# Kernel tuning notes

Hardware: AMD Instinct MI355X
Metric: run time of the kernel (lower is better)

The kernel has to match this reference:

```python
import jax, jax.numpy as jnp
from jax import lax
import numpy as np

B = 16384
D = 32
N_HEADS = 4


def _piece_table():
    base = np.zeros((7, 4, 4), np.int32)
    cells = [
        [(1, 0), (1, 1), (1, 2), (1, 3)],  # I
        [(1, 1), (1, 2), (2, 1), (2, 2)],  # O
        [(1, 1), (2, 0), (2, 1), (2, 2)],  # T
        [(1, 1), (1, 2), (2, 0), (2, 1)],  # S
        [(1, 0), (1, 1), (2, 1), (2, 2)],  # Z
        [(1, 0), (2, 0), (2, 1), (2, 2)],  # J
        [(1, 2), (2, 0), (2, 1), (2, 2)],  # L
    ]
    for i, cs in enumerate(cells):
        for (r, c) in cs:
            base[i, r, c] = 1
    rots = np.stack([np.stack([np.rot90(base[i], k) for k in range(4)]) for i in range(7)])
    p = np.concatenate([rots, np.zeros((1, 4, 4, 4), np.int32)], 0)  # [8,4,4,4]
    return jnp.asarray(p)


def setup_inputs() -> dict:
    key = jax.random.key(0)
    ks = jax.random.split(key, 24)

    def ri(k, n, lo, hi):
        return jax.random.randint(k, (B, n), lo, hi, dtype=jnp.int32)

    t = jnp.concatenate([
        ri(ks[0], 1, 0, 10),   # col0 feature
        ri(ks[1], 1, 2, 8),
        ri(ks[2], 1, 0, 10),   # col2 y pos
        ri(ks[3], 1, 0, 8),    # col3 drop dist
        ri(ks[4], 1, 0, 4),    # col4 rotation
        ri(ks[5], 3, 0, 10),   # cols5-7
        ri(ks[6], 1, 0, 7),    # col8 piece id
        ri(ks[7], 6, 0, 7),    # cols9-14 hold/next
        ri(ks[8], 7, 0, 10),   # cols15-21
        ri(ks[9], 210, 0, 2),  # cols22-231 board
    ], axis=1)

    s = 0.05
    rn = lambda k, shp: jax.random.normal(k, shp, jnp.float32) * s
    return {
        "t": t,
        "piece_table": _piece_table(),
        "conv1_w": rn(ks[10], (6, 3, 5, 5)), "conv1_b": rn(ks[11], (6,)),
        "conv2_w": rn(ks[12], (16, 6, 5, 5)), "conv2_b": rn(ks[13], (16,)),
        "conv3_w": rn(ks[14], (64, 16, 3, 1)), "conv3_b": rn(ks[15], (64,)),
        "lfc1_w": rn(ks[16], (32, 64)), "lfc1_b": rn(ks[17], (32,)),
        "fc_w": rn(ks[18], (32, 8)), "fc_b": rn(ks[19], (32,)),
        "emb": rn(ks[20], (8, D)),
        "in_proj_w": rn(ks[21], (3 * D, D)), "in_proj_b": jnp.zeros((3 * D,), jnp.float32),
        "out_proj_w": rn(ks[22], (D, D)), "out_proj_b": jnp.zeros((D,), jnp.float32),
    }


def _avgpool2(x):
    b, c, h, w = x.shape
    h2, w2 = h // 2, w // 2
    return x[:, :, :h2 * 2, :w2 * 2].reshape(b, c, h2, 2, w2, 2).mean((3, 5))


def _lenet(x, w1, b1, w2, b2, w3, b3, fw, fb):
    dn = ("NCHW", "OIHW", "NCHW")
    x = jax.nn.relu(lax.conv_general_dilated(x, w1, (1, 1), ((2, 2), (2, 2)), dimension_numbers=dn) + b1[None, :, None, None])
    x = _avgpool2(x)                                   # [B,6,11,6]
    x = jax.nn.relu(lax.conv_general_dilated(x, w2, (1, 1), ((0, 0), (0, 0)), dimension_numbers=dn) + b2[None, :, None, None])
    x = _avgpool2(x)                                   # [B,16,3,1]
    x = jax.nn.relu(lax.conv_general_dilated(x, w3, (1, 1), ((0, 0), (0, 0)), dimension_numbers=dn) + b3[None, :, None, None])
    x = x.reshape(-1, 64)
    return jax.nn.relu(x @ fw.T + fb)                  # [B,32]


def _pe():
    pos = jnp.array([0, 0, 1, 2, 3, 4, 5], jnp.float32)[:, None]
    div = jnp.exp(jnp.arange(0, D, 2, dtype=jnp.float32) * (-jnp.log(10000.0) / D))
    s, c = jnp.sin(pos * div), jnp.cos(pos * div)      # [7,16] each
    return jnp.stack([s, c], -1).reshape(7, D)         # interleaved sin/cos


def _mha(q_in, kv, in_w, in_b, out_w, out_b):
    qw, kw, vw = in_w[:D], in_w[D:2 * D], in_w[2 * D:]
    qb, kb, vb = in_b[:D], in_b[D:2 * D], in_b[2 * D:]
    b, lq, _ = q_in.shape
    hd = D // N_HEADS
    q = (q_in @ qw.T + qb).reshape(b, lq, N_HEADS, hd)
    k = (kv @ kw.T + kb).reshape(b, -1, N_HEADS, hd)
    v = (kv @ vw.T + vb).reshape(b, -1, N_HEADS, hd)
    scores = jnp.einsum("bqhd,bkhd->bhqk", q, k) / jnp.sqrt(jnp.float32(hd))
    w = jax.nn.softmax(scores, axis=-1)
    o = jnp.einsum("bhqk,bkhd->bqhd", w, v).reshape(b, lq, D)
    return o @ out_w.T + out_b


def reference(t, piece_table, conv1_w, conv1_b, conv2_w, conv2_b, conv3_w, conv3_b,
              lfc1_w, lfc1_b, fc_w, fc_b, emb, in_proj_w, in_proj_b, out_proj_w, out_proj_b):
    bsz = t.shape[0]
    board = jnp.zeros((bsz, 3, 21, 10), jnp.float32)
    board = board.at[:, 0].set(t[:, 22:232].astype(jnp.float32).reshape(bsz, 21, 10))

    # gather piece grid, extract the 4 filled cells per sample in row-major order
    pieces = piece_table[t[:, 8], t[:, 4]].reshape(bsz, 16)        # [B,16] in {0,1}
    idx = jnp.argsort(1 - pieces, axis=1, stable=True)[:, :4]      # first 4 ones, scan order
    cy, cx = idx // 4, idx % 4
    x = cx + t[:, 1][:, None] - 2
    y = cy + t[:, 2][:, None]
    ny = y + t[:, 3][:, None]
    mask = (y >= 0) & (ny >= 0)
    br = jnp.arange(bsz, dtype=jnp.int32)[:, None]
    y_m = jnp.where(mask, y, -1)
    ny_m = jnp.where(mask, ny, -1)
    board = board.at[br, 1, y_m, x].set(1.0, mode="drop")
    board = board.at[br, 2, ny_m, x].set(1.0, mode="drop")

    board = jnp.pad(board, ((0, 0), (0, 0), (0, 1), (1, 1)), constant_values=1.0)  # [B,3,22,12]

    t9 = jnp.where((t[:, 9] != -1) & (t[:, 6] != 0), t[:, 9], 7)
    hold_next = jnp.concatenate([t[:, 8:9], t9[:, None], t[:, 10:15]], axis=1)     # [B,7]

    b2 = _lenet(board, conv1_w, conv1_b, conv2_w, conv2_b, conv3_w, conv3_b, lfc1_w, lfc1_b)  # [B,32]
    bkv = b2[:, None, :]                                            # [B,1,32]
    p = emb[hold_next] + _pe()[None]                                # [B,7,32]
    a = _mha(p, bkv, in_proj_w, in_proj_b, out_proj_w, out_proj_b)  # [B,7,32]

    xf = jax.nn.relu(t[:, :8].astype(jnp.float32) @ fc_w.T + fc_b)  # [B,32]
    out = jnp.concatenate([xf, a.mean(axis=1), b2], axis=1)         # [B,96]
    return (out, board)
```

## Files before the change

### kernel.cpp

```cpp
#include <hip/hip_runtime.h>
#include <cstddef>


#define BATCH 16384
#define SPB   4
#define NBLK  (BATCH / SPB)
#define RS    18
#define SBE_SZ 432
#define P1OFF  432
#define PCSOFF 800
#define SS2    816

__global__ __launch_bounds__(256)
void cborder_kernel(const float* __restrict__ w1, float* __restrict__ cb)
{
  int i = blockIdx.x * 256 + threadIdx.x;
  if (i >= 1584) return;
  int p = i / 6, o = i - p * 6;
  int y0 = p / 12, x0 = p - y0 * 12;
  float acc = 0.f;
#pragma unroll
  for (int dy = 0; dy < 5; ++dy)
#pragma unroll
    for (int dx = 0; dx < 5; ++dx) {
      int pr = y0 + dy - 2, pc = x0 + dx - 2;
      if (pr >= 0 && pr < 22 && pc >= 0 && pc < 12 &&
          (pr == 21 || pc == 0 || pc == 11)) {
        int k = dy * 5 + dx;
        acc += w1[(o * 3 + 0) * 25 + k] + w1[(o * 3 + 1) * 25 + k]
             + w1[(o * 3 + 2) * 25 + k];
      }
    }
  cb[p * 6 + o] = acc;
}

__global__ __launch_bounds__(256)
void board_model_kernel(const int* __restrict__ t,
                        const int* __restrict__ piece_table,
                        const float* __restrict__ w1, const float* __restrict__ b1,
                        const float* __restrict__ w2, const float* __restrict__ b2w,
                        const float* __restrict__ w3, const float* __restrict__ b3,
                        const float* __restrict__ wf1, const float* __restrict__ bf1,
                        const float* __restrict__ fcw, const float* __restrict__ fcb,
                        const float* __restrict__ ipw, const float* __restrict__ ipb,
                        const float* __restrict__ opw, const float* __restrict__ opb,
                        const float* __restrict__ cbg,
                        float* __restrict__ out,
                        float* __restrict__ out_board)
{
  __shared__ __align__(16) float scr[SPB * SS2];
  __shared__ float w1L[300];
  __shared__ float cbL[1440];

  const int tid  = threadIdx.x;
  const int lane = tid & 63;
  const int wv   = tid >> 6;
  const int bb   = blockIdx.x * SPB;

  for (int i = tid; i < 300; i += 256)
    w1L[i] = w1[(i / 50) * 75 + 25 + (i % 50)];
  for (int i = tid; i < 1440; i += 256) cbL[i] = cbg[i];

  {
    float* W = &scr[wv * SS2];
    int*   pcs = (int*)&scr[wv * SS2 + PCSOFF];
    const int* tr = t + (size_t)(bb + wv) * 232;

    float4* W4 = (float4*)W;
    for (int i = lane; i < 108; i += 64) W4[i] = float4{0.f, 0.f, 0.f, 0.f};

    for (int i = lane; i < 210; i += 64) {
      int r = i / 10, b = i - r * 10;
      W[(r + 2) * RS + b + 5] = (float)tr[22 + i];
    }

    if (lane < 4) {
      const int* pt = piece_table + (tr[8] * 4 + tr[4]) * 16;
      int sel = -1, n1 = 0;
#pragma unroll
      for (int j = 0; j < 16; ++j) { if (pt[j]) { if (n1 == lane) sel = j; ++n1; } }
      if (sel < 0) {
        int n0 = 0, want = lane - n1;
#pragma unroll
        for (int j = 0; j < 16; ++j) if (!pt[j]) { if (n0 == want) { sel = j; break; } ++n0; }
      }
      int cy = sel >> 2, cx = sel & 3;
      int x  = cx + tr[1] - 2;
      int y  = cy + tr[2];
      int ny = y + tr[3];
      bool mask = (y >= 0) && (ny >= 0);
      bool xok  = (x >= 0) && (x < 10);
      bool v1 = mask && xok && (y < 21);
      bool v2 = mask && xok && (ny < 21);
      pcs[2 * lane + 0]       = v1 ? y  : -100;
      pcs[2 * lane + 1]       = x + 1;
      pcs[2 * (lane + 4)]     = v2 ? ny : -100;
      pcs[2 * (lane + 4) + 1] = x + 1;
    }
    __builtin_amdgcn_wave_barrier();

    float* ob = out_board + (size_t)(bb + wv) * 792;
    for (int v = lane; v < 198; v += 64) {
      int j0 = v * 4;
      int ch = j0 / 264, rem = j0 - ch * 264;
      int r = rem / 12, c = rem - r * 12;
      float val[4];
      if (ch == 0) {
#pragma unroll
        for (int d = 0; d < 4; ++d) {
          int cd = c + d;
          val[d] = (r == 21 || cd == 0 || cd == 11) ? 1.f
                 : W[(r + 2) * RS + cd + 4];
        }
      } else {
#pragma unroll
        for (int d = 0; d < 4; ++d) {
          int cd = c + d;
          val[d] = (r == 21 || cd == 0 || cd == 11) ? 1.f : 0.f;
        }
#pragma unroll
        for (int e = 0; e < 4; ++e) {
          int pr = pcs[2 * ((ch - 1) * 4 + e)];
          int pc = pcs[2 * ((ch - 1) * 4 + e) + 1];
          if (pr == r && (unsigned)(pc - c) < 4u) val[pc - c] = 1.f;
        }
      }
      *(float4*)(ob + j0) = float4{val[0], val[1], val[2], val[3]};
    }
  }
  __syncthreads();

  if (lane < 60) {
    int p = lane;
    int r = p / 6, c = p - r * 6;
    const float* Wq  = &scr[wv * SS2];
    const int*   pcs = (const int*)&scr[wv * SS2 + PCSOFF];
    float acc[2][2][6];
#pragma unroll
    for (int i = 0; i < 2; ++i)
#pragma unroll
      for (int j = 0; j < 2; ++j) {
        int pcell = (2 * r + i) * 12 + (2 * c + j);
#pragma unroll
        for (int o = 0; o < 6; ++o)
          acc[i][j][o] = b1[o] + cbL[pcell * 6 + o];
      }

    {
      const float* base = Wq + (2 * r) * RS + (2 * c + 2);
#pragma unroll
      for (int u = 0; u < 6; ++u) {
        float2 a0 = *(const float2*)(base + u * RS);
        float2 a1 = *(const float2*)(base + u * RS + 2);
        float2 a2 = *(const float2*)(base + u * RS + 4);
        float rv[6] = {a0.x, a0.y, a1.x, a1.y, a2.x, a2.y};
#pragma unroll
        for (int i = 0; i < 2; ++i) {
          if (u - i < 0 || u - i > 4) continue;
          const int ky = u - i;
#pragma unroll
          for (int j = 0; j < 2; ++j)
#pragma unroll
            for (int kx = 0; kx < 5; ++kx) {
              float xv = rv[j + kx];
#pragma unroll
              for (int o = 0; o < 6; ++o)
                acc[i][j][o] += xv * w1[o * 75 + ky * 5 + kx];
            }
        }
      }
    }

#pragma unroll
    for (int e = 0; e < 8; ++e) {
      int pr = pcs[2 * e];
      if (pr < 0) continue;
      int pc = pcs[2 * e + 1];
      int chm = e >> 2;
      int dyb = pr + 2 - 2 * r;
      int dxb = pc + 2 - 2 * c;
      if (dyb < 0 || dyb > 5 || dxb < 0 || dxb > 5) continue;
#pragma unroll
      for (int i = 0; i < 2; ++i) {
        int dy = dyb - i;
        if ((unsigned)dy >= 5u) continue;
#pragma unroll
        for (int j = 0; j < 2; ++j) {
          int dx = dxb - j;
          if ((unsigned)dx >= 5u) continue;
#pragma unroll
          for (int o = 0; o < 6; ++o)
            acc[i][j][o] += w1L[(o * 2 + chm) * 25 + dy * 5 + dx];
        }
      }
    }

    float* P1q = &scr[wv * SS2 + P1OFF];
#pragma unroll
    for (int o = 0; o < 6; ++o) {
      float v = fmaxf(acc[0][0][o], 0.f) + fmaxf(acc[0][1][o], 0.f)
              + fmaxf(acc[1][0][o], 0.f) + fmaxf(acc[1][1][o], 0.f);
      P1q[o * 61 + p] = 0.25f * v;
    }
  }
  __syncthreads();

  const int wvu = __builtin_amdgcn_readfirstlane(wv);

  if (lane < 48) {
    int q = lane / 12, p = lane - q * 12;
    int r = p >> 1, c = p & 1;
    const float* P1q = &scr[q * SS2 + P1OFF];
    float a4[4];
#pragma unroll
    for (int oo = 0; oo < 4; ++oo) a4[oo] = b2w[4 * wvu + oo];
    for (int ic = 0; ic < 6; ++ic)
#pragma unroll
      for (int kr = 0; kr < 5; ++kr) {
        float xv[5];
#pragma unroll
        for (int kc = 0; kc < 5; ++kc)
          xv[kc] = P1q[ic * 61 + (r + kr) * 6 + c + kc];
#pragma unroll
        for (int kc = 0; kc < 5; ++kc)
#pragma unroll
          for (int oo = 0; oo < 4; ++oo)
            a4[oo] += xv[kc] * w2[(((4 * wvu + oo) * 6 + ic) * 5 + kr) * 5 + kc];
      }
    float* C2q = &scr[q * SS2];
#pragma unroll
    for (int oo = 0; oo < 4; ++oo)
      C2q[(4 * wvu + oo) * 12 + p] = fmaxf(a4[oo], 0.f);
  }
  __syncthreads();

  {
    const int q = wvu;
    float* S = &scr[q * SS2];

    if (lane < 48) {
      int o = lane / 3, pr = lane - o * 3;
      float v = 0.25f * (S[o * 12 + 4 * pr] + S[o * 12 + 4 * pr + 1]
                       + S[o * 12 + 4 * pr + 2] + S[o * 12 + 4 * pr + 3]);
      S[192 + lane] = v;
    }
    __builtin_amdgcn_wave_barrier();

    {
      int o = lane;
      float acc = b3[o];
#pragma unroll
      for (int k = 0; k < 48; ++k) acc += S[192 + k] * w3[o * 48 + k];
      S[240 + o] = fmaxf(acc, 0.f);
    }
    __builtin_amdgcn_wave_barrier();

    {
      int j = lane & 31, h = lane >> 5;
      float part = 0.f;
#pragma unroll
      for (int kk = 0; kk < 32; ++kk) {
        int k = 32 * h + kk;
        part += S[240 + k] * wf1[j * 64 + k];
      }
      part += __shfl_xor(part, 32, 64);
      if (h == 0) {
        float acc = fmaxf(bf1[j] + part, 0.f);
        S[304 + j] = acc;
        out[(size_t)(bb + q) * 96 + 64 + j] = acc;
      }
    }
    __builtin_amdgcn_wave_barrier();

    {
      int j = lane & 31;
      if (lane < 32) {
        float acc = ipb[64 + j];
#pragma unroll
        for (int k = 0; k < 32; ++k) acc += S[304 + k] * ipw[(64 + j) * 32 + k];
        S[336 + j] = acc;
      } else {
        const int* tr = t + (size_t)(bb + q) * 232;
        float acc = fcb[j];
#pragma unroll
        for (int k = 0; k < 8; ++k) acc += (float)tr[k] * fcw[j * 8 + k];
        out[(size_t)(bb + q) * 96 + j] = fmaxf(acc, 0.f);
      }
    }
    __builtin_amdgcn_wave_barrier();

    if (lane < 32) {
      int j = lane;
      float acc = opb[j];
#pragma unroll
      for (int k = 0; k < 32; ++k) acc += S[336 + k] * opw[j * 32 + k];
      out[(size_t)(bb + q) * 96 + 32 + j] = acc;
    }
  }
}

extern "C" void kernel_launch(void* const* d_in, const int* in_sizes, int n_in,
                              void* d_out, int out_size, void* d_ws, size_t ws_size,
                              hipStream_t stream) {
  const int*   t   = (const int*)d_in[0];
  const int*   pt  = (const int*)d_in[1];
  const float* w1  = (const float*)d_in[2];
  const float* b1  = (const float*)d_in[3];
  const float* w2  = (const float*)d_in[4];
  const float* b2w = (const float*)d_in[5];
  const float* w3  = (const float*)d_in[6];
  const float* b3  = (const float*)d_in[7];
  const float* wf1 = (const float*)d_in[8];
  const float* bf1 = (const float*)d_in[9];
  const float* fcw = (const float*)d_in[10];
  const float* fcb = (const float*)d_in[11];
  const float* ipw = (const float*)d_in[13];
  const float* ipb = (const float*)d_in[14];
  const float* opw = (const float*)d_in[15];
  const float* opb = (const float*)d_in[16];

  float* out       = (float*)d_out;
  float* out_board = out + (size_t)BATCH * 96;
  float* cbg       = (float*)d_ws;

  hipLaunchKernelGGL(cborder_kernel, dim3(7), dim3(256), 0, stream, w1, cbg);
  hipLaunchKernelGGL(board_model_kernel, dim3(NBLK), dim3(256), 0, stream,
                     t, pt, w1, b1, w2, b2w, w3, b3, wf1, bf1, fcw, fcb,
                     ipw, ipb, opw, opb, cbg, out, out_board);
}
```

Before: 197.7 us.

## Use ballot piece lookup, row bitmasks, vectorized loads, and lighter barriers

Several local changes to the fused kernel. The board is loaded as int2 pairs. The piece cell selection uses a wave ballot plus ctz instead of serial loops. Per-row piece bitmasks, built with LDS atomics, replace the per-element scan of piece cells when writing the output board. The w1 weights in LDS are relaid so the 6 output channels sit contiguously, the conv2 input-channel loop is fully unrolled, and __syncthreads is replaced with a raw lgkmcnt wait plus s_barrier. Together these aim to cut ALU and synchronization overhead. The trade-offs are more register pressure from the unrolling, and inline asm barriers that do not wait on vector memory counters.

```diff
diff --git a/kernel.cpp b/kernel.cpp
--- a/kernel.cpp
+++ b/kernel.cpp
@@ -10,6 +10,8 @@
 #define P1OFF  432
 #define PCSOFF 800
 #define SS2    816
+
+#define BSYNC() asm volatile("s_waitcnt lgkmcnt(0)\ns_barrier" ::: "memory")
 
 __global__ __launch_bounds__(256)
 void cborder_kernel(const float* __restrict__ w1, float* __restrict__ cb)
@@ -57,53 +59,63 @@
   const int wv   = tid >> 6;
   const int bb   = blockIdx.x * SPB;
 
-  for (int i = tid; i < 300; i += 256)
-    w1L[i] = w1[(i / 50) * 75 + 25 + (i % 50)];
+  for (int i = tid; i < 300; i += 256) {
+    int o = i % 6, tt = i / 6, m = tt / 25, tp = tt - m * 25;
+    w1L[i] = w1[(o * 3 + m + 1) * 25 + tp];
+  }
   for (int i = tid; i < 1440; i += 256) cbL[i] = cbg[i];
 
   {
     float* W = &scr[wv * SS2];
     int*   pcs = (int*)&scr[wv * SS2 + PCSOFF];
+    int*   bmi = (int*)&scr[wv * SS2 + P1OFF];
     const int* tr = t + (size_t)(bb + wv) * 232;
 
     float4* W4 = (float4*)W;
     for (int i = lane; i < 108; i += 64) W4[i] = float4{0.f, 0.f, 0.f, 0.f};
-
-    for (int i = lane; i < 210; i += 64) {
-      int r = i / 10, b = i - r * 10;
-      W[(r + 2) * RS + b + 5] = (float)tr[22 + i];
-    }
-
-    if (lane < 4) {
+    if (lane < 44) bmi[lane] = 0;
+
+    {
+      const int2* cp = (const int2*)(tr + 22);
+      for (int v = lane; v < 105; v += 64) {
+        int2 cv = cp[v];
+        int i0 = v * 2;
+        int r = i0 / 10, b = i0 - r * 10;
+        W[(r + 2) * RS + b + 5] = (float)cv.x;
+        W[(r + 2) * RS + b + 6] = (float)cv.y;
+      }
+    }
+
+    {
       const int* pt = piece_table + (tr[8] * 4 + tr[4]) * 16;
-      int sel = -1, n1 = 0;
-#pragma unroll
-      for (int j = 0; j < 16; ++j) { if (pt[j]) { if (n1 == lane) sel = j; ++n1; } }
-      if (sel < 0) {
-        int n0 = 0, want = lane - n1;
-#pragma unroll
-        for (int j = 0; j < 16; ++j) if (!pt[j]) { if (n0 == want) { sel = j; break; } ++n0; }
-      }
-      int cy = sel >> 2, cx = sel & 3;
-      int x  = cx + tr[1] - 2;
-      int y  = cy + tr[2];
-      int ny = y + tr[3];
-      bool mask = (y >= 0) && (ny >= 0);
-      bool xok  = (x >= 0) && (x < 10);
-      bool v1 = mask && xok && (y < 21);
-      bool v2 = mask && xok && (ny < 21);
-      pcs[2 * lane + 0]       = v1 ? y  : -100;
-      pcs[2 * lane + 1]       = x + 1;
-      pcs[2 * (lane + 4)]     = v2 ? ny : -100;
-      pcs[2 * (lane + 4) + 1] = x + 1;
+      int ptv = (lane < 16) ? pt[lane] : 0;
+      unsigned long long bal = __ballot(ptv != 0);
+      if (lane < 4) {
+        unsigned x = (unsigned)bal & 0xffffu;
+        for (int k = 0; k < lane; ++k) x &= x - 1;
+        int sel = __builtin_ctz(x);
+        int cy = sel >> 2, cx = sel & 3;
+        int xx = cx + tr[1] - 2;
+        int y  = cy + tr[2];
+        int ny = y + tr[3];
+        bool mask = (y >= 0) && (ny >= 0);
+        bool xok  = (xx >= 0) && (xx < 10);
+        bool v1 = mask && xok && (y < 21);
+        bool v2 = mask && xok && (ny < 21);
+        pcs[2 * lane + 0]       = v1 ? y  : -100;
+        pcs[2 * lane + 1]       = xx + 1;
+        pcs[2 * (lane + 4)]     = v2 ? ny : -100;
+        pcs[2 * (lane + 4) + 1] = xx + 1;
+        if (v1) atomicOr(&bmi[y],       1 << (xx + 1));
+        if (v2) atomicOr(&bmi[22 + ny], 1 << (xx + 1));
+      }
     }
     __builtin_amdgcn_wave_barrier();
 
     float* ob = out_board + (size_t)(bb + wv) * 792;
     for (int v = lane; v < 198; v += 64) {
-      int j0 = v * 4;
-      int ch = j0 / 264, rem = j0 - ch * 264;
-      int r = rem / 12, c = rem - r * 12;
+      int ch = v / 66, w = v - ch * 66;
+      int r = w / 3, c = (w - r * 3) * 4;
       float val[4];
       if (ch == 0) {
 #pragma unroll
@@ -113,22 +125,17 @@
                  : W[(r + 2) * RS + cd + 4];
         }
       } else {
+        int bits = bmi[(ch - 1) * 22 + r];
 #pragma unroll
         for (int d = 0; d < 4; ++d) {
           int cd = c + d;
-          val[d] = (r == 21 || cd == 0 || cd == 11) ? 1.f : 0.f;
+          val[d] = (r == 21 || cd == 0 || cd == 11 || ((bits >> cd) & 1)) ? 1.f : 0.f;
         }
-#pragma unroll
-        for (int e = 0; e < 4; ++e) {
-          int pr = pcs[2 * ((ch - 1) * 4 + e)];
-          int pc = pcs[2 * ((ch - 1) * 4 + e) + 1];
-          if (pr == r && (unsigned)(pc - c) < 4u) val[pc - c] = 1.f;
-        }
-      }
-      *(float4*)(ob + j0) = float4{val[0], val[1], val[2], val[3]};
-    }
-  }
-  __syncthreads();
+      }
+      *(float4*)(ob + v * 4) = float4{val[0], val[1], val[2], val[3]};
+    }
+  }
+  BSYNC();
 
   if (lane < 60) {
     int p = lane;
@@ -188,9 +195,10 @@
         for (int j = 0; j < 2; ++j) {
           int dx = dxb - j;
           if ((unsigned)dx >= 5u) continue;
+          const float* wp = &w1L[(chm * 25 + dy * 5 + dx) * 6];
 #pragma unroll
           for (int o = 0; o < 6; ++o)
-            acc[i][j][o] += w1L[(o * 2 + chm) * 25 + dy * 5 + dx];
+            acc[i][j][o] += wp[o];
         }
       }
     }
@@ -203,7 +211,7 @@
       P1q[o * 61 + p] = 0.25f * v;
     }
   }
-  __syncthreads();
+  BSYNC();
 
   const int wvu = __builtin_amdgcn_readfirstlane(wv);
 
@@ -214,6 +222,7 @@
     float a4[4];
 #pragma unroll
     for (int oo = 0; oo < 4; ++oo) a4[oo] = b2w[4 * wvu + oo];
+#pragma unroll
     for (int ic = 0; ic < 6; ++ic)
 #pragma unroll
       for (int kr = 0; kr < 5; ++kr) {
@@ -232,7 +241,7 @@
     for (int oo = 0; oo < 4; ++oo)
       C2q[(4 * wvu + oo) * 12 + p] = fmaxf(a4[oo], 0.f);
   }
-  __syncthreads();
+  BSYNC();
 
   {
     const int q = wvu;
```

New measurement: 196.9 us. About the same (-0.4%).
